# Optimization experiments

Measured on AMD Instinct MI355X. Metric: run time of the kernel, lower is better.

The kernel has to match this reference:

```python
import math
import jax, jax.numpy as jnp
import numpy as np

NUM_HEADS = 4
HEAD_DIM = 384


def reshape_fortran(x, shape):
    # column-major (Fortran) reshape, matching the torch reverse-permute trick
    x = jnp.transpose(x, tuple(reversed(range(x.ndim))))
    x = x.reshape(tuple(reversed(shape)))
    return jnp.transpose(x, tuple(reversed(range(len(shape)))))


def rel_pos_rotate(data):
    # data: [b, n_heads, L=2M-1, S] -> [b, n_heads, S, S]
    data = jnp.transpose(data, (0, 2, 3, 1))  # [b, d0=L, d1=S, d2=H]
    b, d0, d1, d2 = data.shape
    data = jnp.concatenate([data, jnp.zeros((b, d1, d1, d2), data.dtype)], axis=1)
    data = reshape_fortran(data, (b, (d0 + d1) * d1, 1, d2))
    data = data[:, :(d1 + d0 - 1) * d1]
    data = reshape_fortran(data, (b, d0 + d1 - 1, d1, d2))
    n = d0 // 2
    data = jnp.swapaxes(data[:, n:n + d1], 1, 2)  # [b, d1, d1, d2]
    return jnp.transpose(data, (0, 3, 1, 2))      # [b, H, S, S]


def setup_inputs() -> dict:
    key = jax.random.key(0)
    ks = jax.random.split(key, 5)
    B, S, D = 4, 920, 1536
    M = 920
    return {
        "hidden_states": jax.random.normal(ks[0], (B, S, D), jnp.float32),
        "q_w": jax.random.normal(ks[1], (D, NUM_HEADS * HEAD_DIM), jnp.float32) * 0.02,
        "k_w": jax.random.normal(ks[2], (D, NUM_HEADS * HEAD_DIM), jnp.float32) * 0.02,
        "v_w": jax.random.normal(ks[3], (D, NUM_HEADS * HEAD_DIM), jnp.float32) * 0.02,
        "dist_emb": jax.random.normal(ks[4], (2 * M - 1, HEAD_DIM), jnp.float32) * 0.02,
    }


def reference(hidden_states, q_w, k_w, v_w, dist_emb):
    B, S, D = hidden_states.shape

    def heads(x):  # [B,S,H*hd] -> [B,H,S,hd]
        return jnp.transpose(x.reshape(B, S, NUM_HEADS, HEAD_DIM), (0, 2, 1, 3))

    # query is pre-scaled by 1/sqrt(head_dim), matching the torch code
    q = heads((hidden_states @ q_w) / math.sqrt(HEAD_DIM))
    k = heads(hidden_states @ k_w)
    v = heads(hidden_states @ v_w)

    scores = jnp.einsum("bhqd,bhkd->bhqk", q, k)  # [B,H,S,S]
    # relative position scores: [B,H,L,S] then skew-rotated into [B,H,S,S]
    rel = jnp.einsum("ld,bhsd->bhls", dist_emb, q)
    scores = scores + rel_pos_rotate(rel)

    probs = jax.nn.softmax(scores, axis=-1)
    ctx = jnp.einsum("bhqk,bhkd->bhqd", probs, v)  # [B,H,S,hd]
    ctx = jnp.transpose(ctx, (0, 2, 1, 3)).reshape(B, S, NUM_HEADS * HEAD_DIM)
    return ctx
```

## Files before the change

### kernel.cpp

```cpp
#include <hip/hip_runtime.h>
#include <cstdint>
#include <cstddef>

#define SEQ   920
#define DM    1536
#define DH    384
#define NHD   4
#define NB    4
#define NBH   16
#define MTOK  3680
#define NREL  1839

typedef short          bf16x8 __attribute__((ext_vector_type(8)));
typedef float          f32x4  __attribute__((ext_vector_type(4)));
typedef unsigned short u16x4  __attribute__((ext_vector_type(4)));
typedef unsigned short u16x8  __attribute__((ext_vector_type(8)));

__device__ __forceinline__ unsigned short f2bf(float f){
  union{float f; unsigned u;} v; v.f = f;
  unsigned r = v.u + 0x7FFFu + ((v.u >> 16) & 1u);
  return (unsigned short)(r >> 16);
}
__device__ __forceinline__ float bf2f(unsigned short h){
  union{unsigned u; float f;} v; v.u = ((unsigned)h) << 16;
  return v.f;
}
__device__ __forceinline__ f32x4 mfma_bf16(bf16x8 a, bf16x8 b, f32x4 c){
  return __builtin_amdgcn_mfma_f32_16x16x32_bf16(a, b, c, 0, 0, 0);
}
__device__ __forceinline__ void gload_lds16(const void* g, void* l){
  __builtin_amdgcn_global_load_lds((const __attribute__((address_space(1))) void*)g,
                                   (__attribute__((address_space(3))) void*)l, 16, 0, 0);
}

__global__ __launch_bounds__(256) void k_prep(const float* __restrict__ X,
                                              const float* __restrict__ de,
                                              const float* __restrict__ qw,
                                              const float* __restrict__ kw,
                                              const float* __restrict__ vw,
                                              unsigned short* __restrict__ Xb,
                                              unsigned short* __restrict__ Eb,
                                              unsigned short* __restrict__ Wt){
  __shared__ float t[32][33];
  int bid = blockIdx.x;
  if(bid < 6912){
    int z = bid / 2304, rem = bid % 2304;
    int k0 = (rem % 48) * 32, n0 = (rem / 48) * 32;
    const float* w = z == 0 ? qw : (z == 1 ? kw : vw);
    int tx = threadIdx.x & 31, ty = threadIdx.x >> 5;
    #pragma unroll
    for(int j = 0; j < 4; j++)
      t[ty*4+j][tx] = w[(size_t)(k0 + ty*4 + j) * DM + n0 + tx];
    __syncthreads();
    #pragma unroll
    for(int j = 0; j < 4; j++)
      Wt[(size_t)(z*DM + n0 + ty*4 + j) * DM + k0 + tx] = f2bf(t[tx][ty*4+j]);
  } else if(bid < 6912 + 2048){
    int i = ((bid - 6912) * 256 + threadIdx.x) * 4;
    const int n = MTOK*DM, stride = 2048 * 256 * 4;
    for(; i + 3 < n; i += stride){
      f32x4 v = *(const f32x4*)(X + i);
      u16x4 o; o.x = f2bf(v.x); o.y = f2bf(v.y); o.z = f2bf(v.z); o.w = f2bf(v.w);
      *(u16x4*)(Xb + i) = o;
    }
  } else {
    int i = ((bid - 6912 - 2048) * 256 + threadIdx.x) * 4;
    if(i + 3 < NREL*DH){
      f32x4 v = *(const f32x4*)(de + i);
      u16x4 o; o.x = f2bf(v.x); o.y = f2bf(v.y); o.z = f2bf(v.z); o.w = f2bf(v.w);
      *(u16x4*)(Eb + i) = o;
    }
  }
}

template<class Epi>
__device__ __forceinline__ void gemm384(const unsigned short* __restrict__ A, int lda, int Amax,
                                        const unsigned short* __restrict__ B, int ldb, int Bmax,
                                        int K, int m0, int n0, Epi epi){
  __shared__ char lds[147456];
  char* ldsA = lds;
  char* ldsB = lds + 98304;
  const int tid = threadIdx.x;
  const int w = tid >> 6, l = tid & 63;
  const int lg = l >> 4, lo = l & 15;
  const int wm = w >> 1, wn = w & 1;

  const int gcol = ((tid & 7) ^ ((tid >> 3) & 7)) * 16;
  const char* gA[6]; const char* gB[3];
  #pragma unroll
  for(int u = 0; u < 6; u++){
    int ar = m0 + u*64 + (tid >> 3); ar = ar < Amax ? ar : Amax - 1;
    gA[u] = (const char*)A + (size_t)ar*lda*2 + gcol;
  }
  #pragma unroll
  for(int v = 0; v < 3; v++){
    int br = n0 + v*64 + (tid >> 3); br = br < Bmax ? br : Bmax - 1;
    gB[v] = (const char*)B + (size_t)br*ldb*2 + gcol;
  }
  auto stage_all = [&](int kt, int s){
    size_t koff = (size_t)kt * 128;
    #pragma unroll
    for(int u = 0; u < 6; u++)
      gload_lds16(gA[u] + koff, ldsA + s*49152 + u*8192 + tid*16);
    #pragma unroll
    for(int v = 0; v < 3; v++)
      gload_lds16(gB[v] + koff, ldsB + s*24576 + v*8192 + tid*16);
  };

  f32x4 acc[6][6] = {};
  const int sw = (lo & 7) << 4;
  const int nk = K >> 6;

  stage_all(0, 0);
  asm volatile("s_waitcnt vmcnt(0)" ::: "memory");
  __builtin_amdgcn_s_barrier();

  for(int t = 0; t < nk; t++){
    const int s = t & 1, sn = s ^ 1;
    const bool pf = (t + 1 < nk);
    const char* Ab = ldsA + s*49152;
    const char* Bb = ldsB + s*24576;
    if(pf) stage_all(t + 1, sn);

    bf16x8 b0[6], b1[6], a0[3], a1[3];
    #pragma unroll
    for(int fj = 0; fj < 6; fj++){
      b0[fj] = *(const bf16x8*)(Bb + (wn*96 + fj*16 + lo)*128 + ((lg*16) ^ sw));
      b1[fj] = *(const bf16x8*)(Bb + (wn*96 + fj*16 + lo)*128 + ((64 + lg*16) ^ sw));
    }
    #pragma unroll
    for(int fi = 0; fi < 3; fi++){
      a0[fi] = *(const bf16x8*)(Ab + (wm*96 + fi*16 + lo)*128 + ((lg*16) ^ sw));
      a1[fi] = *(const bf16x8*)(Ab + (wm*96 + fi*16 + lo)*128 + ((64 + lg*16) ^ sw));
    }
    __builtin_amdgcn_s_setprio(1);
    #pragma unroll
    for(int fi = 0; fi < 3; fi++)
      #pragma unroll
      for(int fj = 0; fj < 6; fj++)
        acc[fi][fj] = mfma_bf16(a0[fi], b0[fj], acc[fi][fj]);
    #pragma unroll
    for(int fi = 0; fi < 3; fi++)
      #pragma unroll
      for(int fj = 0; fj < 6; fj++)
        acc[fi][fj] = mfma_bf16(a1[fi], b1[fj], acc[fi][fj]);
    __builtin_amdgcn_s_setprio(0);

    #pragma unroll
    for(int fi = 0; fi < 3; fi++){
      a0[fi] = *(const bf16x8*)(Ab + (wm*96 + (fi+3)*16 + lo)*128 + ((lg*16) ^ sw));
      a1[fi] = *(const bf16x8*)(Ab + (wm*96 + (fi+3)*16 + lo)*128 + ((64 + lg*16) ^ sw));
    }
    __builtin_amdgcn_s_setprio(1);
    #pragma unroll
    for(int fi = 0; fi < 3; fi++)
      #pragma unroll
      for(int fj = 0; fj < 6; fj++)
        acc[fi+3][fj] = mfma_bf16(a0[fi], b0[fj], acc[fi+3][fj]);
    #pragma unroll
    for(int fi = 0; fi < 3; fi++)
      #pragma unroll
      for(int fj = 0; fj < 6; fj++)
        acc[fi+3][fj] = mfma_bf16(a1[fi], b1[fj], acc[fi+3][fj]);
    __builtin_amdgcn_s_setprio(0);

    if(pf){
      asm volatile("s_waitcnt vmcnt(0)" ::: "memory");
      __builtin_amdgcn_s_barrier();
    }
  }

  #pragma unroll
  for(int fi = 0; fi < 6; fi++)
    #pragma unroll
    for(int fj = 0; fj < 6; fj++){
      int m = m0 + wm*96 + fi*16 + lg*4;
      int n = n0 + wn*96 + fj*16 + lo;
      epi(m, n, acc[fi][fj]);
    }
}

template<class Epi>
__device__ __forceinline__ void gemm192(const unsigned short* __restrict__ A, int lda, int Amax,
                                        const unsigned short* __restrict__ B, int ldb, int Bmax,
                                        int K, int m0, int n0, Epi epi){
  __shared__ unsigned short As[3*192*64];
  __shared__ unsigned short Bs[3*192*64];
  const int tid = threadIdx.x;
  const int w = tid >> 6, l = tid & 63;
  const int lg = l >> 4, lo = l & 15;
  const int wm = w >> 2, wn = w & 3;

  const char* ga[3]; const char* gb[3];
  #pragma unroll
  for(int r = 0; r < 3; r++){
    int row = r*64 + (tid >> 3);
    int gslot = (tid & 7) ^ (row & 7);
    int ar = m0 + row; ar = ar < Amax ? ar : Amax - 1;
    ga[r] = (const char*)A + (size_t)ar*lda*2 + gslot*16;
    int br = n0 + row; br = br < Bmax ? br : Bmax - 1;
    gb[r] = (const char*)B + (size_t)br*ldb*2 + gslot*16;
  }
  const int ldst = tid * 16;

  auto stage_pair = [&](int kt, int slot, int r){
    size_t koff = (size_t)kt * 128;
    gload_lds16(ga[r] + koff, (char*)As + slot*24576 + r*8192 + ldst);
    gload_lds16(gb[r] + koff, (char*)Bs + slot*24576 + r*8192 + ldst);
  };

  f32x4 acc[6][3] = {};
  const int sw = (lo & 7) << 4;
  const int nk = (2*K + 127) >> 7;
  const int tb = 2*K - (nk - 1)*128;
  const bool keep0 = (lg*16) < tb;
  const bool keep1 = (64 + lg*16) < tb;

  #pragma unroll
  for(int r = 0; r < 3; r++) stage_pair(0, 0, r);
  #pragma unroll
  for(int r = 0; r < 3; r++) stage_pair(1, 1, r);
  asm volatile("s_waitcnt vmcnt(6)" ::: "memory");
  __builtin_amdgcn_s_barrier();

  int st = 0;
  for(int t = 0; t < nk; t++){
    const bool last = (t == nk - 1);
    const bool pf = (t + 2 < nk);
    const int s2 = st + 2 >= 3 ? st - 1 : st + 2;
    const char* Ab = (const char*)As + st*24576;
    const char* Bb = (const char*)Bs + st*24576;

    bf16x8 bfr[3][2], afr[2][2];

    #pragma unroll
    for(int fj = 0; fj < 3; fj++){
      int row = wn*48 + fj*16 + lo;
      #pragma unroll
      for(int kk = 0; kk < 2; kk++)
        bfr[fj][kk] = *(const bf16x8*)(Bb + row*128 + ((kk*64 + lg*16) ^ sw));
    }
    #pragma unroll
    for(int fi = 0; fi < 2; fi++){
      int row = wm*96 + fi*16 + lo;
      #pragma unroll
      for(int kk = 0; kk < 2; kk++)
        afr[fi][kk] = *(const bf16x8*)(Ab + row*128 + ((kk*64 + lg*16) ^ sw));
    }
    if(pf) stage_pair(t + 2, s2, 0);
    if(last){
      #pragma unroll
      for(int fi = 0; fi < 2; fi++){
        if(!keep0) afr[fi][0] = bf16x8{};
        if(!keep1) afr[fi][1] = bf16x8{};
      }
    }
    __builtin_amdgcn_s_barrier();
    asm volatile("s_waitcnt lgkmcnt(0)" ::: "memory");
    __builtin_amdgcn_s_setprio(1);
    #pragma unroll
    for(int kk = 0; kk < 2; kk++)
      #pragma unroll
      for(int fi = 0; fi < 2; fi++)
        #pragma unroll
        for(int fj = 0; fj < 3; fj++)
          acc[fi][fj] = mfma_bf16(afr[fi][kk], bfr[fj][kk], acc[fi][fj]);
    __builtin_amdgcn_s_setprio(0);
    __builtin_amdgcn_s_barrier();

    #pragma unroll
    for(int fi = 0; fi < 2; fi++){
      int row = wm*96 + (fi + 2)*16 + lo;
      #pragma unroll
      for(int kk = 0; kk < 2; kk++)
        afr[fi][kk] = *(const bf16x8*)(Ab + row*128 + ((kk*64 + lg*16) ^ sw));
    }
    if(pf) stage_pair(t + 2, s2, 1);
    if(last){
      #pragma unroll
      for(int fi = 0; fi < 2; fi++){
        if(!keep0) afr[fi][0] = bf16x8{};
        if(!keep1) afr[fi][1] = bf16x8{};
      }
    }
    __builtin_amdgcn_s_barrier();
    asm volatile("s_waitcnt lgkmcnt(0)" ::: "memory");
    __builtin_amdgcn_s_setprio(1);
    #pragma unroll
    for(int kk = 0; kk < 2; kk++)
      #pragma unroll
      for(int fi = 0; fi < 2; fi++)
        #pragma unroll
        for(int fj = 0; fj < 3; fj++)
          acc[fi + 2][fj] = mfma_bf16(afr[fi][kk], bfr[fj][kk], acc[fi + 2][fj]);
    __builtin_amdgcn_s_setprio(0);
    __builtin_amdgcn_s_barrier();

    #pragma unroll
    for(int fi = 0; fi < 2; fi++){
      int row = wm*96 + (fi + 4)*16 + lo;
      #pragma unroll
      for(int kk = 0; kk < 2; kk++)
        afr[fi][kk] = *(const bf16x8*)(Ab + row*128 + ((kk*64 + lg*16) ^ sw));
    }
    if(pf){
      stage_pair(t + 2, s2, 2);
      asm volatile("s_waitcnt vmcnt(6)" ::: "memory");
    } else if(t + 1 < nk){
      asm volatile("s_waitcnt vmcnt(0)" ::: "memory");
    }
    if(last){
      #pragma unroll
      for(int fi = 0; fi < 2; fi++){
        if(!keep0) afr[fi][0] = bf16x8{};
        if(!keep1) afr[fi][1] = bf16x8{};
      }
    }
    __builtin_amdgcn_s_barrier();
    asm volatile("s_waitcnt lgkmcnt(0)" ::: "memory");
    __builtin_amdgcn_s_setprio(1);
    #pragma unroll
    for(int kk = 0; kk < 2; kk++)
      #pragma unroll
      for(int fi = 0; fi < 2; fi++)
        #pragma unroll
        for(int fj = 0; fj < 3; fj++)
          acc[fi + 4][fj] = mfma_bf16(afr[fi][kk], bfr[fj][kk], acc[fi + 4][fj]);
    __builtin_amdgcn_s_setprio(0);
    __builtin_amdgcn_s_barrier();

    st = st + 1 >= 3 ? 0 : st + 1;
  }

  #pragma unroll
  for(int fi = 0; fi < 6; fi++)
    #pragma unroll
    for(int fj = 0; fj < 3; fj++){
      int m = m0 + wm*96 + fi*16 + lg*4;
      int n = n0 + wn*48 + fj*16 + lo;
      epi(m, n, acc[fi][fj]);
    }
}

template<class Epi>
__device__ __forceinline__ void gemm256(const unsigned short* __restrict__ A, int lda, int Amax,
                                        const unsigned short* __restrict__ B, int ldb, int Bmax,
                                        int K, int m0, int n0, Epi epi){
  __shared__ char lds[131072];
  char* ldsA = lds;
  char* ldsB = lds + 65536;
  const int tid = threadIdx.x;
  const int w = tid >> 6, l = tid & 63;
  const int lg = l >> 4, lo = l & 15;
  const int wm = w >> 2, wn = w & 3;

  const int gcol = ((tid & 7) ^ ((tid >> 3) & 7)) * 16;
  const char* gA[2][2]; const char* gB[2][2];
  #pragma unroll
  for(int u = 0; u < 2; u++)
    #pragma unroll
    for(int j = 0; j < 2; j++){
      int ar = m0 + u*128 + j*64 + (tid >> 3); ar = ar < Amax ? ar : Amax - 1;
      gA[u][j] = (const char*)A + (size_t)ar*lda*2 + gcol;
      int br = n0 + u*128 + j*64 + (tid >> 3); br = br < Bmax ? br : Bmax - 1;
      gB[u][j] = (const char*)B + (size_t)br*ldb*2 + gcol;
    }
  auto stageA = [&](int kt, int s, int u){
    size_t koff = (size_t)kt * 128;
    #pragma unroll
    for(int j = 0; j < 2; j++)
      gload_lds16(gA[u][j] + koff, ldsA + s*32768 + u*16384 + j*8192 + tid*16);
  };
  auto stageB = [&](int kt, int s, int u){
    size_t koff = (size_t)kt * 128;
    #pragma unroll
    for(int j = 0; j < 2; j++)
      gload_lds16(gB[u][j] + koff, ldsB + s*32768 + u*16384 + j*8192 + tid*16);
  };

  f32x4 acc[2][4][4] = {};
  const int sw = (lo & 7) << 4;
  const int nk = K >> 6;

  stageB(0, 0, 0); stageB(0, 0, 1); stageA(0, 0, 0); stageA(0, 0, 1);
  asm volatile("s_waitcnt vmcnt(2)" ::: "memory");
  __builtin_amdgcn_s_barrier();

  for(int t = 0; t < nk; t++){
    const int s = t & 1, sn = s ^ 1;
    const bool pf = (t + 1 < nk);
    const char* Ab = ldsA + s*32768;
    const char* Bb = ldsB + s*32768;
    bf16x8 b0[4], b1[4], ar[4];

    #pragma unroll
    for(int fj = 0; fj < 4; fj++)
      b0[fj] = *(const bf16x8*)(Bb + (wn*64 + fj*16 + lo)*128 + ((lg*16) ^ sw));
    #pragma unroll
    for(int fi = 0; fi < 4; fi++)
      ar[fi] = *(const bf16x8*)(Ab + (wm*64 + fi*16 + lo)*128 + ((lg*16) ^ sw));
    if(pf) stageB(t + 1, sn, 0);
    __builtin_amdgcn_s_barrier();
    asm volatile("s_waitcnt lgkmcnt(0)" ::: "memory");
    __builtin_amdgcn_s_setprio(1);
    #pragma unroll
    for(int fi = 0; fi < 4; fi++)
      #pragma unroll
      for(int fj = 0; fj < 4; fj++)
        acc[0][fi][fj] = mfma_bf16(ar[fi], b0[fj], acc[0][fi][fj]);
    __builtin_amdgcn_s_setprio(0);

    #pragma unroll
    for(int fj = 0; fj < 4; fj++)
      b1[fj] = *(const bf16x8*)(Bb + (wn*64 + fj*16 + lo)*128 + ((64 + lg*16) ^ sw));
    #pragma unroll
    for(int fi = 0; fi < 4; fi++)
      ar[fi] = *(const bf16x8*)(Ab + (wm*64 + fi*16 + lo)*128 + ((64 + lg*16) ^ sw));
    if(pf){ stageB(t + 1, sn, 1);
            asm volatile("s_waitcnt vmcnt(4)" ::: "memory"); }
    else  { asm volatile("s_waitcnt vmcnt(0)" ::: "memory"); }
    __builtin_amdgcn_s_barrier();
    asm volatile("s_waitcnt lgkmcnt(0)" ::: "memory");
    __builtin_amdgcn_s_setprio(1);
    #pragma unroll
    for(int fi = 0; fi < 4; fi++)
      #pragma unroll
      for(int fj = 0; fj < 4; fj++)
        acc[0][fi][fj] = mfma_bf16(ar[fi], b1[fj], acc[0][fi][fj]);
    __builtin_amdgcn_s_setprio(0);

    #pragma unroll
    for(int fi = 0; fi < 4; fi++)
      ar[fi] = *(const bf16x8*)(Ab + (128 + wm*64 + fi*16 + lo)*128 + ((lg*16) ^ sw));
    if(pf) stageA(t + 1, sn, 0);
    __builtin_amdgcn_s_barrier();
    asm volatile("s_waitcnt lgkmcnt(0)" ::: "memory");
    __builtin_amdgcn_s_setprio(1);
    #pragma unroll
    for(int fi = 0; fi < 4; fi++)
      #pragma unroll
      for(int fj = 0; fj < 4; fj++)
        acc[1][fi][fj] = mfma_bf16(ar[fi], b0[fj], acc[1][fi][fj]);
    __builtin_amdgcn_s_setprio(0);

    #pragma unroll
    for(int fi = 0; fi < 4; fi++)
      ar[fi] = *(const bf16x8*)(Ab + (128 + wm*64 + fi*16 + lo)*128 + ((64 + lg*16) ^ sw));
    if(pf){ stageA(t + 1, sn, 1);
            asm volatile("s_waitcnt vmcnt(2)" ::: "memory"); }
    __builtin_amdgcn_s_barrier();
    asm volatile("s_waitcnt lgkmcnt(0)" ::: "memory");
    __builtin_amdgcn_s_setprio(1);
    #pragma unroll
    for(int fi = 0; fi < 4; fi++)
      #pragma unroll
      for(int fj = 0; fj < 4; fj++)
        acc[1][fi][fj] = mfma_bf16(ar[fi], b1[fj], acc[1][fi][fj]);
    __builtin_amdgcn_s_setprio(0);
  }

  #pragma unroll
  for(int lh = 0; lh < 2; lh++)
    #pragma unroll
    for(int fi = 0; fi < 4; fi++)
      #pragma unroll
      for(int fj = 0; fj < 4; fj++){
        int m = m0 + lh*128 + wm*64 + fi*16 + lg*4;
        int n = n0 + wn*64 + fj*16 + lo;
        epi(m, n, acc[lh][fi][fj]);
      }
}

__global__ __launch_bounds__(512, 2) void k_proj(const unsigned short* __restrict__ X,
                                                 const unsigned short* __restrict__ Wt,
                                                 unsigned short* __restrict__ Qb,
                                                 unsigned short* __restrict__ Kb,
                                                 unsigned short* __restrict__ Vt){
  int bid = blockIdx.x;
  int wg  = (bid & 7) * 30 + (bid >> 3);
  int m0 = (wg % 10) * 384, n0 = (wg / 10) * 192;
  gemm384(X, DM, MTOK, Wt, DM, 3*DM, DM, m0, n0,
    [=] __device__ (int m, int n, f32x4 v4){
      if(m >= MTOK) return;
      int which = n / DM, r = n % DM, h = r / DH, d = r % DH;
      int b = m / SEQ, s = m % SEQ;
      int bh = b * NHD + h;
      if(which == 2){
        u16x4 o;
        o.x = f2bf(v4.x); o.y = f2bf(v4.y); o.z = f2bf(v4.z); o.w = f2bf(v4.w);
        *(u16x4*)(Vt + ((size_t)bh*DH + d)*SEQ + s) = o;
      } else if(which == 0){
        #pragma unroll
        for(int i = 0; i < 4; i++)
          Qb[((size_t)bh*SEQ + s + i)*DH + d] = f2bf(v4[i] * 0.05103103630798287f);
      } else {
        #pragma unroll
        for(int i = 0; i < 4; i++)
          Kb[((size_t)bh*SEQ + s + i)*DH + d] = f2bf(v4[i]);
      }
    });
}

__global__ __launch_bounds__(512) void k_rel(const unsigned short* __restrict__ Qb,
                                             const unsigned short* __restrict__ E,
                                             unsigned short* __restrict__ relS){
  int m0 = blockIdx.x * 192, n0 = blockIdx.y * 192;
  int s0 = m0 % SEQ;
  int qlo = s0, qhi = s0 + 191;
  if(qhi >= SEQ){ qlo = 0; qhi = SEQ - 1; }
  if(n0 + 191 < 919 - qhi || n0 > 1838 - qlo) return;
  gemm192(Qb, DH, NBH*SEQ, E, DH, NREL, DH, m0, n0,
    [=] __device__ (int m, int n, f32x4 v4){
      #pragma unroll
      for(int i = 0; i < 4; i++){
        int mi = m + i;
        if(mi >= NBH*SEQ) continue;
        int q = mi % SEQ;
        int j = n - 919 + q;
        if(j < 0 || j >= SEQ) continue;
        relS[(size_t)mi*SEQ + j] = f2bf(v4[i]);
      }
    });
}

__global__ __launch_bounds__(512, 2) void k_sgemm(const unsigned short* __restrict__ Qb,
                                                  const unsigned short* __restrict__ Kb,
                                                  unsigned short* __restrict__ P,
                                                  float* __restrict__ rs2){
  __shared__ float rsLds[256];
  if(threadIdx.x < 256) rsLds[threadIdx.x] = 0.f;
  int bid = blockIdx.x;
  int wg = (bid & 7) * 32 + (bid >> 3);
  int bh = wg >> 4, r = wg & 15;
  int m0 = (r & 3) * 256, n0 = (r >> 2) * 256;
  const unsigned short* A = Qb + (size_t)bh*SEQ*DH;
  const unsigned short* B = Kb + (size_t)bh*SEQ*DH;
  unsigned short* Pbh = P + (size_t)bh*SEQ*SEQ;
  const int lo = threadIdx.x & 15;
  gemm256(A, DH, SEQ, B, DH, SEQ, DH, m0, n0,
    [=] __device__ (int m, int n, f32x4 v4){
      float s[4];
      #pragma unroll
      for(int i = 0; i < 4; i++){
        int mi = m + i;
        float p = 0.f;
        if(mi < SEQ && n < SEQ){
          size_t off = (size_t)mi*SEQ + n;
          p = __expf(v4[i] + bf2f(Pbh[off]));
          Pbh[off] = f2bf(p);
        }
        s[i] = p;
      }
      #pragma unroll
      for(int i = 0; i < 4; i++){
        float v = s[i];
        v += __shfl_xor(v, 1); v += __shfl_xor(v, 2);
        v += __shfl_xor(v, 4); v += __shfl_xor(v, 8);
        if(lo == 0) atomicAdd(&rsLds[m - m0 + i], v);
      }
    });
  __syncthreads();
  if(threadIdx.x < 256){
    int row = m0 + threadIdx.x;
    if(row < SEQ) rs2[(((size_t)(n0 >> 8))*NBH + bh)*SEQ + row] = rsLds[threadIdx.x];
  }
}

__global__ __launch_bounds__(512) void k_pv(const unsigned short* __restrict__ P,
                                            const unsigned short* __restrict__ Vt,
                                            const float* __restrict__ rs2,
                                            float* __restrict__ out){
  int bid = blockIdx.x;
  int idp = (bid & 7) * 20 + (bid >> 3);
  int bh = idp / 10, r = idp % 10;
  int m0 = (r % 5) * 192, n0 = (r / 5) * 192;
  const unsigned short* A = P  + (size_t)bh*SEQ*SEQ;
  const unsigned short* B = Vt + (size_t)bh*DH*SEQ;
  const int b = bh >> 2, h = bh & 3;
  gemm192(A, SEQ, SEQ, B, SEQ, DH, SEQ, m0, n0,
    [=] __device__ (int m, int n, f32x4 v4){
      #pragma unroll
      for(int i = 0; i < 4; i++){
        int mi = m + i;
        if(mi >= SEQ) continue;
        float den = rs2[(size_t)bh*SEQ + mi]
                  + rs2[((size_t)1*NBH + bh)*SEQ + mi]
                  + rs2[((size_t)2*NBH + bh)*SEQ + mi]
                  + rs2[((size_t)3*NBH + bh)*SEQ + mi];
        out[((size_t)(b*SEQ + mi))*DM + h*DH + n] = v4[i] / den;
      }
    });
}

extern "C" void kernel_launch(void* const* d_in, const int* in_sizes, int n_in,
                              void* d_out, int out_size, void* d_ws, size_t ws_size,
                              hipStream_t stream){
  const float* X  = (const float*)d_in[0];
  const float* qw = (const float*)d_in[1];
  const float* kw = (const float*)d_in[2];
  const float* vw = (const float*)d_in[3];
  const float* de = (const float*)d_in[4];
  float* out = (float*)d_out;
  char* ws = (char*)d_ws;

  unsigned short* Qb   = (unsigned short*)ws;
  unsigned short* Kb   = (unsigned short*)(ws + 11304960);
  unsigned short* Vt   = (unsigned short*)(ws + 22609920);
  unsigned short* relS = (unsigned short*)(ws + 33914880);
  unsigned short* Eb   = (unsigned short*)(ws + 60999680);
  unsigned short* Xb   = (unsigned short*)(ws + 33914880);
  unsigned short* Wt   = (unsigned short*)(ws + 45219840);
  float*          rs2  = (float*)(ws + 60999680);

  k_prep<<<dim3(9650), dim3(256), 0, stream>>>(X, de, qw, kw, vw, Xb, Eb, Wt);
  k_proj<<<dim3(240), dim3(512), 0, stream>>>(Xb, Wt, Qb, Kb, Vt);
  k_rel<<<dim3(77,10), dim3(512), 0, stream>>>(Qb, Eb, relS);
  k_sgemm<<<dim3(256), dim3(512), 0, stream>>>(Qb, Kb, relS, rs2);
  k_pv<<<dim3(160), dim3(512), 0, stream>>>(relS, Vt, rs2, out);
}
```

Before: 208.7 us.

## Split A/B tile prefetch and use partial vmcnt waits in GEMM mainloop

Splits the double-buffered global-to-LDS staging into separate A and B loads and uses counted vmcnt waits instead of draining all loads, so one operand's prefetch can still be in flight while the other is consumed. It also reorders LDS fragment loads: all A fragments first, then B per k-half, with MFMAs over the full 6x6 tile. This adds an extra barrier per iteration and raises live fragment registers.

After: 210.5 us. Within noise of the previous version (+0.9%).

```diff
diff --git a/kernel.cpp b/kernel.cpp
--- a/kernel.cpp
+++ b/kernel.cpp
@@ -97,11 +97,14 @@
     int br = n0 + v*64 + (tid >> 3); br = br < Bmax ? br : Bmax - 1;
     gB[v] = (const char*)B + (size_t)br*ldb*2 + gcol;
   }
-  auto stage_all = [&](int kt, int s){
+  auto stageA = [&](int kt, int s){
     size_t koff = (size_t)kt * 128;
     #pragma unroll
     for(int u = 0; u < 6; u++)
       gload_lds16(gA[u] + koff, ldsA + s*49152 + u*8192 + tid*16);
+  };
+  auto stageB = [&](int kt, int s){
+    size_t koff = (size_t)kt * 128;
     #pragma unroll
     for(int v = 0; v < 3; v++)
       gload_lds16(gB[v] + koff, ldsB + s*24576 + v*8192 + tid*16);
@@ -111,8 +114,9 @@
   const int sw = (lo & 7) << 4;
   const int nk = K >> 6;
 
-  stage_all(0, 0);
-  asm volatile("s_waitcnt vmcnt(0)" ::: "memory");
+  stageA(0, 0);
+  stageB(0, 0);
+  asm volatile("s_waitcnt vmcnt(3)" ::: "memory");
   __builtin_amdgcn_s_barrier();
 
   for(int t = 0; t < nk; t++){
@@ -120,52 +124,43 @@
     const bool pf = (t + 1 < nk);
     const char* Ab = ldsA + s*49152;
     const char* Bb = ldsB + s*24576;
-    if(pf) stage_all(t + 1, sn);
-
-    bf16x8 b0[6], b1[6], a0[3], a1[3];
-    #pragma unroll
-    for(int fj = 0; fj < 6; fj++){
-      b0[fj] = *(const bf16x8*)(Bb + (wn*96 + fj*16 + lo)*128 + ((lg*16) ^ sw));
-      b1[fj] = *(const bf16x8*)(Bb + (wn*96 + fj*16 + lo)*128 + ((64 + lg*16) ^ sw));
-    }
-    #pragma unroll
-    for(int fi = 0; fi < 3; fi++){
+    bf16x8 a0[6], a1[6], b0[6], b1[6];
+
+    #pragma unroll
+    for(int fi = 0; fi < 6; fi++){
       a0[fi] = *(const bf16x8*)(Ab + (wm*96 + fi*16 + lo)*128 + ((lg*16) ^ sw));
       a1[fi] = *(const bf16x8*)(Ab + (wm*96 + fi*16 + lo)*128 + ((64 + lg*16) ^ sw));
     }
-    __builtin_amdgcn_s_setprio(1);
-    #pragma unroll
-    for(int fi = 0; fi < 3; fi++)
+    if(pf) stageA(t + 1, sn);
+
+    if(pf){ asm volatile("s_waitcnt vmcnt(6)" ::: "memory"); }
+    else  { asm volatile("s_waitcnt vmcnt(0)" ::: "memory"); }
+    __builtin_amdgcn_s_barrier();
+    #pragma unroll
+    for(int fj = 0; fj < 6; fj++)
+      b0[fj] = *(const bf16x8*)(Bb + (wn*96 + fj*16 + lo)*128 + ((lg*16) ^ sw));
+    if(pf) stageB(t + 1, sn);
+    __builtin_amdgcn_s_setprio(1);
+    #pragma unroll
+    for(int fi = 0; fi < 6; fi++)
       #pragma unroll
       for(int fj = 0; fj < 6; fj++)
         acc[fi][fj] = mfma_bf16(a0[fi], b0[fj], acc[fi][fj]);
-    #pragma unroll
-    for(int fi = 0; fi < 3; fi++)
+    __builtin_amdgcn_s_setprio(0);
+
+    #pragma unroll
+    for(int fj = 0; fj < 6; fj++)
+      b1[fj] = *(const bf16x8*)(Bb + (wn*96 + fj*16 + lo)*128 + ((64 + lg*16) ^ sw));
+    __builtin_amdgcn_s_setprio(1);
+    #pragma unroll
+    for(int fi = 0; fi < 6; fi++)
       #pragma unroll
       for(int fj = 0; fj < 6; fj++)
         acc[fi][fj] = mfma_bf16(a1[fi], b1[fj], acc[fi][fj]);
     __builtin_amdgcn_s_setprio(0);
 
-    #pragma unroll
-    for(int fi = 0; fi < 3; fi++){
-      a0[fi] = *(const bf16x8*)(Ab + (wm*96 + (fi+3)*16 + lo)*128 + ((lg*16) ^ sw));
-      a1[fi] = *(const bf16x8*)(Ab + (wm*96 + (fi+3)*16 + lo)*128 + ((64 + lg*16) ^ sw));
-    }
-    __builtin_amdgcn_s_setprio(1);
-    #pragma unroll
-    for(int fi = 0; fi < 3; fi++)
-      #pragma unroll
-      for(int fj = 0; fj < 6; fj++)
-        acc[fi+3][fj] = mfma_bf16(a0[fi], b0[fj], acc[fi+3][fj]);
-    #pragma unroll
-    for(int fi = 0; fi < 3; fi++)
-      #pragma unroll
-      for(int fj = 0; fj < 6; fj++)
-        acc[fi+3][fj] = mfma_bf16(a1[fi], b1[fj], acc[fi+3][fj]);
-    __builtin_amdgcn_s_setprio(0);
-
     if(pf){
-      asm volatile("s_waitcnt vmcnt(0)" ::: "memory");
+      asm volatile("s_waitcnt vmcnt(3)" ::: "memory");
       __builtin_amdgcn_s_barrier();
     }
   }
```
